# Performance work log

Measured on AMD Instinct MI355X. Metric: run time of the kernel, lower is better.

The kernel has to match this reference:

```python
import jax, jax.numpy as jnp
import numpy as np

PSZ = 3      # patch_size
TOPK = 2     # topk candidates
EPS = 1e-12  # F.normalize eps


def extract_patches(x, psz, stride):
    """Torch unfold-style patch extraction: (B,C,H,W) -> (B, nH*nW, C, psz, psz)."""
    B, C, H, W = x.shape
    nH = (H - psz) // stride + 1
    nW = (W - psz) // stride + 1
    slices = []
    for di in range(psz):          # fixed 3x3 loop, not a data-dim loop
        for dj in range(psz):
            slices.append(x[:, :, di:di + (nH - 1) * stride + 1:stride,
                                  dj:dj + (nW - 1) * stride + 1:stride])
    p = jnp.stack(slices, axis=-1)                      # (B,C,nH,nW,psz*psz)
    p = p.reshape(B, C, nH, nW, psz, psz)
    p = p.transpose(0, 2, 3, 1, 4, 5).reshape(B, nH * nW, C, psz, psz)
    return p


def l2_normalize(x, axis):
    n = jnp.sqrt(jnp.sum(x * x, axis=axis, keepdims=True))
    return x / jnp.maximum(n, EPS)


def setup_inputs() -> dict:
    key = jax.random.key(0)
    k1, k2 = jax.random.split(key)
    pred_style = jax.random.normal(k1, (2, 128, 48, 48), dtype=jnp.float32)
    target_style = jax.random.normal(k2, (2 * TOPK, 128, 48, 48), dtype=jnp.float32)
    return {"pred_style": pred_style, "target_style": target_style}


def reference(pred_style, target_style):
    B = pred_style.shape[0]
    # raw patches (used for the final MSE / gather)
    tp = extract_patches(target_style, PSZ, 1)   # (B*TOPK, nT, C, 3, 3)
    pp = extract_patches(pred_style, PSZ, 1)     # (B, nQ, C, 3, 3)
    nT = tp.shape[1]

    # matching is done on channel-normalized features (F.normalize dim=1 / dim=2)
    p1n = extract_patches(l2_normalize(pred_style, axis=1), PSZ, 1)  # (B,nQ,C,3,3)
    tpn = l2_normalize(tp, axis=2).reshape(B, TOPK, nT, *tp.shape[2:])

    # cosine cross-correlation == conv with candidate patches as filters
    scores = jnp.einsum('bqcij,bkncij->bknq', p1n, tpn)  # (B,TOPK,nT,nQ)->(B,TOPK,nQ) reduce below

    sv = jnp.max(scores, axis=2)      # (B, TOPK, nQ) best value per candidate set
    si = jnp.argmax(scores, axis=2)   # (B, TOPK, nQ) best spatial idx per k
    k_idx = jnp.argmax(sv, axis=1)    # (B, nQ) best k per query position
    spatial = jnp.take_along_axis(si, k_idx[:, None, :], axis=1)[:, 0]  # (B, nQ)

    tpr = tp.reshape(B, TOPK, nT, *tp.shape[2:])
    bi = jnp.arange(B)[:, None]
    gathered = tpr[bi, k_idx, spatial]  # (B, nQ, C, 3, 3)

    return jnp.mean((pp - gathered) ** 2)
```

## Files before the change

### kernel.cpp

```cpp
#include <hip/hip_runtime.h>
#include <hip/hip_bf16.h>

typedef unsigned short u16;
typedef __attribute__((ext_vector_type(8))) short short8;
typedef __attribute__((ext_vector_type(4))) float f32x4;
typedef __attribute__((ext_vector_type(4))) unsigned int u32x4;

#define CC    128
#define WW    48
#define HW2   2304
#define NHW   46
#define NQ    2116
#define NPIX  2304
#define DSTRIDE ((size_t)NPIX * NPIX + 64)
#define BATCH 2
#define MT    126
#define NTC   254

__device__ __forceinline__ u16 f2bf(float f) {
  union { float f; unsigned u; } x; x.f = f;
  unsigned r = (x.u + 0x7fffu + ((x.u >> 16) & 1u)) >> 16;
  return (u16)r;
}
__device__ __forceinline__ float b2f(u16 v) {
  union { unsigned u; float f; } x; x.u = ((unsigned)v) << 16;
  return x.f;
}

__global__ __launch_bounds__(256) void k_norm(const float* __restrict__ pred,
                                              const float* __restrict__ targ,
                                              u16* __restrict__ PnT, u16* __restrict__ TnT) {
  const int img = blockIdx.y;
  const int p0  = blockIdx.x * 64;
  const int tid = threadIdx.x;
  const float* src = img < 2 ? pred + (size_t)img * CC * HW2
                             : targ + (size_t)(img - 2) * CC * HW2;
  u16* out = img < 2 ? PnT + (size_t)img * NPIX * CC
                     : TnT + (size_t)(img - 2) * NPIX * CC;

  __shared__ float sT[64][129];
  __shared__ float sInv[64];

  #pragma unroll
  for (int it = 0; it < 32; ++it) {
    int idx = it * 256 + tid;
    int c = idx >> 6, p = idx & 63;
    sT[p][c] = src[(size_t)c * HW2 + p0 + p];
  }
  __syncthreads();
  if (tid < 64) {
    float s = 0.f;
    for (int c = 0; c < CC; ++c) { float v = sT[tid][c]; s += v * v; }
    sInv[tid] = 1.0f / fmaxf(sqrtf(s), 1e-12f);
  }
  __syncthreads();
  #pragma unroll
  for (int it = 0; it < 4; ++it) {
    int cid = it * 256 + tid;
    int p = cid >> 4, g = cid & 15;
    int r = p0 + p;
    int sc = (g & ~7) | ((g & 7) ^ (r & 7));
    float inv = sInv[p];
    unsigned pack[4];
    #pragma unroll
    for (int e = 0; e < 8; ++e) {
      float v = sT[p][sc * 8 + e] * inv;
      if ((e & 1) == 0) pack[e >> 1] = (unsigned)f2bf(v);
      else              pack[e >> 1] |= ((unsigned)f2bf(v)) << 16;
    }
    u32x4 o; o.x = pack[0]; o.y = pack[1]; o.z = pack[2]; o.w = pack[3];
    *reinterpret_cast<u32x4*>(out + (size_t)r * CC + g * 8) = o;
  }
}

__global__ __launch_bounds__(512) void k_pixdotH(const u16* __restrict__ PnT, const u16* __restrict__ TnT,
                                                 u16* __restrict__ H) {
  __shared__ u16 buf[49152];
  u16* sA = buf;
  u16* sB = buf + 16384;
  const int nt = blockIdx.x, mt = blockIdx.y, s = blockIdx.z;
  const int tid = threadIdx.x, lane = tid & 63, wid = tid >> 6;
  const int wm = wid >> 2, wn = wid & 3;
  const int r15 = lane & 15, g16 = lane >> 4;
  const int m0 = mt * MT, n0 = nt * NTC;

  const u16* Ab = PnT + (size_t)(s >> 1) * NPIX * CC;
  const u16* Bb = TnT + (size_t)s * NPIX * CC;
  u16* Hs = H + (size_t)s * DSTRIDE;

  #pragma unroll
  for (int i = 0; i < 4; ++i) {
    int sl = i * 512 + tid;
    int row = m0 + (sl >> 4); row = row < 2303 ? row : 2303;
    __builtin_amdgcn_global_load_lds(
      (const __attribute__((address_space(1))) unsigned*)(Ab + (size_t)row * CC + (sl & 15) * 8),
      (__attribute__((address_space(3))) unsigned*)&sA[sl * 8], 16, 0, 0);
  }
  #pragma unroll
  for (int i = 0; i < 8; ++i) {
    int sl = i * 512 + tid;
    int row = n0 + (sl >> 4); row = row < 2303 ? row : 2303;
    __builtin_amdgcn_global_load_lds(
      (const __attribute__((address_space(1))) unsigned*)(Bb + (size_t)row * CC + (sl & 15) * 8),
      (__attribute__((address_space(3))) unsigned*)&sB[sl * 8], 16, 0, 0);
  }

  f32x4 acc[4][4];
  const f32x4 z4 = {0.f, 0.f, 0.f, 0.f};
  #pragma unroll
  for (int i = 0; i < 4; ++i)
    #pragma unroll
    for (int j = 0; j < 4; ++j) acc[i][j] = z4;

  asm volatile("s_waitcnt vmcnt(0)" ::: "memory");
  __builtin_amdgcn_s_barrier();

  const int arow0 = wm * 64 + r15;
  const int brow0 = wn * 64 + r15;
  #pragma unroll
  for (int ks = 0; ks < 4; ++ks) {
    const int c = ks * 4 + g16;
    short8 af[4], bfv[4];
    #pragma unroll
    for (int mi = 0; mi < 4; ++mi) {
      int row = arow0 + mi * 16;
      int gr = m0 + row;
      af[mi] = *reinterpret_cast<const short8*>(
        &sA[row * 128 + (c >> 3) * 64 + (((c & 7) ^ (gr & 7)) * 8)]);
    }
    #pragma unroll
    for (int ni = 0; ni < 4; ++ni) {
      int row = brow0 + ni * 16;
      int gr = n0 + row;
      bfv[ni] = *reinterpret_cast<const short8*>(
        &sB[row * 128 + (c >> 3) * 64 + (((c & 7) ^ (gr & 7)) * 8)]);
    }
    __builtin_amdgcn_s_setprio(1);
    #pragma unroll
    for (int mi = 0; mi < 4; ++mi)
      #pragma unroll
      for (int ni = 0; ni < 4; ++ni)
        acc[mi][ni] = __builtin_amdgcn_mfma_f32_16x16x32_bf16(af[mi], bfv[ni], acc[mi][ni], 0, 0, 0);
    __builtin_amdgcn_s_setprio(0);
  }

  __syncthreads();
  u16* Dt = buf;
  #pragma unroll
  for (int mi = 0; mi < 4; ++mi)
    #pragma unroll
    for (int ni = 0; ni < 4; ++ni) {
      int col = wn * 64 + ni * 16 + r15;
      #pragma unroll
      for (int rg = 0; rg < 4; ++rg) {
        int row = wm * 64 + mi * 16 + g16 * 4 + rg;
        Dt[row * 256 + col] = f2bf(acc[mi][ni][rg]);
      }
    }
  __syncthreads();

  for (int t = tid; t < 4032; t += 512) {
    int rr = t >> 5, c8 = t & 31;
    int grow = m0 + rr;
    if (grow >= 2302) continue;
    int lcol = c8 * 8;
    int lim = 254 - lcol;
    int glim = 2302 - (n0 + lcol);
    lim = lim < glim ? lim : glim;
    if (lim <= 0) continue;
    int base = rr * 256 + lcol;
    short8 a0 = *reinterpret_cast<const short8*>(&Dt[base]);
    short8 b0 = *reinterpret_cast<const short8*>(&Dt[base + 256]);
    short8 b1 = *reinterpret_cast<const short8*>(&Dt[base + 264]);
    short8 c0 = *reinterpret_cast<const short8*>(&Dt[base + 512]);
    short8 c1 = *reinterpret_cast<const short8*>(&Dt[base + 520]);
    short8 s1v = __builtin_shufflevector(b0, b1, 1, 2, 3, 4, 5, 6, 7, 8);
    short8 s2v = __builtin_shufflevector(c0, c1, 2, 3, 4, 5, 6, 7, 8, 9);
    unsigned pack[4];
    #pragma unroll
    for (int e = 0; e < 8; ++e) {
      float f = b2f((u16)a0[e]) + b2f((u16)s1v[e]) + b2f((u16)s2v[e]);
      if ((e & 1) == 0) pack[e >> 1] = (unsigned)f2bf(f);
      else              pack[e >> 1] |= ((unsigned)f2bf(f)) << 16;
    }
    u16* dst = Hs + (size_t)grow * NPIX + n0 + lcol;
    int nd = lim >= 8 ? 4 : ((lim + 1) >> 1);
    #pragma unroll
    for (int d = 0; d < 4; ++d)
      if (d < nd) *reinterpret_cast<unsigned*>(dst + 2 * d) = pack[d];
  }
}

__global__ __launch_bounds__(512) void k_stencil(const u16* __restrict__ H,
                                                 const float* __restrict__ pred,
                                                 const float* __restrict__ targ,
                                                 float* __restrict__ msep) {
  const int bid = blockIdx.x;
  const int b = bid >= NQ ? 1 : 0;
  const int orig = bid - b * NQ;
  const int xcd = orig & 7, pos = orig >> 3;
  const int q = (xcd < 4 ? xcd * 265 : 1060 + (xcd - 4) * 264) + pos;

  const int tid = threadIdx.x, lane = tid & 63, wid = tid >> 6;
  const int qy = q / NHW, qx = q - qy * NHW;
  const int qp = qy * WW + qx;

  float best = -3.0e38f; int bidx = 0x7fffffff;
  #pragma unroll
  for (int it = 0; it < 2; ++it) {
    int t = it * 512 + tid;
    if (t < 552) {
      int kc = t / 276; int rem = t - kc * 276;
      int ny = rem / 6, cx = rem - ny * 6;
      const u16* Hs = H + (size_t)(b * 2 + kc) * DSTRIDE;
      int colb = ny * 48 + cx * 8;
      short8 t0 = *reinterpret_cast<const short8*>(Hs + (size_t)qp * NPIX + colb);
      short8 t1 = *reinterpret_cast<const short8*>(Hs + (size_t)(qp + 48) * NPIX + colb + 48);
      short8 t2 = *reinterpret_cast<const short8*>(Hs + (size_t)(qp + 96) * NPIX + colb + 96);
      int nbase = kc * NQ + ny * NHW + cx * 8;
      #pragma unroll
      for (int e = 0; e < 8; ++e) {
        float sc = b2f((u16)t0[e]) + b2f((u16)t1[e]) + b2f((u16)t2[e]);
        int n = nbase + e;
        bool take = (cx * 8 + e < NHW) &&
                    ((sc > best) || (sc == best && n < bidx));
        best = take ? sc : best;
        bidx = take ? n : bidx;
      }
    }
  }
  #pragma unroll
  for (int off = 1; off < 64; off <<= 1) {
    float ov = __shfl_xor(best, off, 64);
    int   oi = __shfl_xor(bidx, off, 64);
    bool take = (ov > best) || (ov == best && oi < bidx);
    best = take ? ov : best;
    bidx = take ? oi : bidx;
  }

  __shared__ float sv[8]; __shared__ int si[8];
  __shared__ float red[512];
  if (lane == 0) { sv[wid] = best; si[wid] = bidx; }
  __syncthreads();
  float fb = sv[0]; int fi = si[0];
  #pragma unroll
  for (int wv = 1; wv < 8; ++wv) {
    bool take = (sv[wv] > fb) || (sv[wv] == fb && si[wv] < fi);
    fb = take ? sv[wv] : fb;
    fi = take ? si[wv] : fi;
  }

  int nkc = fi >= NQ ? 1 : 0;
  int ns = fi - nkc * NQ;
  int ny = ns / NHW, nx = ns - ny * NHW;
  const float* P = pred + (size_t)b * CC * HW2;
  const float* T = targ + (size_t)(b * 2 + nkc) * CC * HW2;
  float ssum = 0.f;
  for (int i = tid; i < CC * 9; i += 512) {
    int c = i / 9, sp = i - 9 * c;
    int di = sp / 3, dj = sp - 3 * di;
    float d = P[(size_t)c * HW2 + (qy + di) * WW + qx + dj]
            - T[(size_t)c * HW2 + (ny + di) * WW + nx + dj];
    ssum += d * d;
  }
  red[tid] = ssum; __syncthreads();
  for (int st = 256; st > 0; st >>= 1) { if (tid < st) red[tid] += red[tid + st]; __syncthreads(); }
  if (tid == 0) msep[b * NQ + q] = red[0];
}

__global__ void k_final(const float* __restrict__ msep, float* __restrict__ out) {
  int t = threadIdx.x;
  float s = 0.f;
  for (int i = t; i < BATCH * NQ; i += 256) s += msep[i];
  __shared__ float red[256];
  red[t] = s; __syncthreads();
  for (int st = 128; st > 0; st >>= 1) { if (t < st) red[t] += red[t + st]; __syncthreads(); }
  if (t == 0) out[0] = red[0] * (1.0f / 4875264.0f);
}

extern "C" void kernel_launch(void* const* d_in, const int* in_sizes, int n_in,
                              void* d_out, int out_size, void* d_ws, size_t ws_size,
                              hipStream_t stream) {
  const float* pred = (const float*)d_in[0];
  const float* targ = (const float*)d_in[1];
  char* ws = (char*)d_ws;

  size_t offP = 0;
  size_t offT = offP + (size_t)2 * NPIX * CC * 2;
  size_t offH = offT + (size_t)4 * NPIX * CC * 2;
  size_t offM = offH + (size_t)4 * DSTRIDE * 2;

  u16*   PnT  = (u16*)(ws + offP);
  u16*   TnT  = (u16*)(ws + offT);
  u16*   Hbuf = (u16*)(ws + offH);
  float* msep = (float*)(ws + offM);

  k_norm<<<dim3(36, 6), 256, 0, stream>>>(pred, targ, PnT, TnT);
  k_pixdotH<<<dim3(10, 19, 4), 512, 0, stream>>>(PnT, TnT, Hbuf);
  k_stencil<<<dim3(BATCH * NQ), 512, 0, stream>>>(Hbuf, pred, targ, msep);
  k_final<<<1, 256, 0, stream>>>(msep, (float*)d_out);
}
```

Baseline: 77.50 us.

## Shrink pixdot N-tile to fit two blocks per CU; use shuffle reduction in stencil

The pixel-dot GEMM kernel's N tile drops from 254 to 190 columns. Each wave now computes 64x48 instead of 64x64, and LDS use falls from 96KB to 80KB, so with launch_bounds(512,2) two blocks can be resident per CU. The grid grows from 10 to 13 N-tiles, which means more blocks and more halo recomputation, and the edge store count is adjusted. Separately, the stencil kernel's 512-entry LDS tree reduction is replaced by wave shuffles plus an 8-entry combine, removing many barriers.

```diff
diff --git a/kernel.cpp b/kernel.cpp
--- a/kernel.cpp
+++ b/kernel.cpp
@@ -15,7 +15,8 @@
 #define DSTRIDE ((size_t)NPIX * NPIX + 64)
 #define BATCH 2
 #define MT    126
-#define NTC   254
+#define NTC   190
+#define DTS   200
 
 __device__ __forceinline__ u16 f2bf(float f) {
   union { float f; unsigned u; } x; x.f = f;
@@ -73,9 +74,9 @@
   }
 }
 
-__global__ __launch_bounds__(512) void k_pixdotH(const u16* __restrict__ PnT, const u16* __restrict__ TnT,
-                                                 u16* __restrict__ H) {
-  __shared__ u16 buf[49152];
+__global__ __launch_bounds__(512, 2) void k_pixdotH(const u16* __restrict__ PnT, const u16* __restrict__ TnT,
+                                                    u16* __restrict__ H) {
+  __shared__ u16 buf[40960];
   u16* sA = buf;
   u16* sB = buf + 16384;
   const int nt = blockIdx.x, mt = blockIdx.y, s = blockIdx.z;
@@ -97,7 +98,7 @@
       (__attribute__((address_space(3))) unsigned*)&sA[sl * 8], 16, 0, 0);
   }
   #pragma unroll
-  for (int i = 0; i < 8; ++i) {
+  for (int i = 0; i < 6; ++i) {
     int sl = i * 512 + tid;
     int row = n0 + (sl >> 4); row = row < 2303 ? row : 2303;
     __builtin_amdgcn_global_load_lds(
@@ -105,22 +106,22 @@
       (__attribute__((address_space(3))) unsigned*)&sB[sl * 8], 16, 0, 0);
   }
 
-  f32x4 acc[4][4];
+  f32x4 acc[4][3];
   const f32x4 z4 = {0.f, 0.f, 0.f, 0.f};
   #pragma unroll
   for (int i = 0; i < 4; ++i)
     #pragma unroll
-    for (int j = 0; j < 4; ++j) acc[i][j] = z4;
+    for (int j = 0; j < 3; ++j) acc[i][j] = z4;
 
   asm volatile("s_waitcnt vmcnt(0)" ::: "memory");
   __builtin_amdgcn_s_barrier();
 
   const int arow0 = wm * 64 + r15;
-  const int brow0 = wn * 64 + r15;
+  const int brow0 = wn * 48 + r15;
   #pragma unroll
   for (int ks = 0; ks < 4; ++ks) {
     const int c = ks * 4 + g16;
-    short8 af[4], bfv[4];
+    short8 af[4], bfv[3];
     #pragma unroll
     for (int mi = 0; mi < 4; ++mi) {
       int row = arow0 + mi * 16;
@@ -129,7 +130,7 @@
         &sA[row * 128 + (c >> 3) * 64 + (((c & 7) ^ (gr & 7)) * 8)]);
     }
     #pragma unroll
-    for (int ni = 0; ni < 4; ++ni) {
+    for (int ni = 0; ni < 3; ++ni) {
       int row = brow0 + ni * 16;
       int gr = n0 + row;
       bfv[ni] = *reinterpret_cast<const short8*>(
@@ -139,7 +140,7 @@
     #pragma unroll
     for (int mi = 0; mi < 4; ++mi)
       #pragma unroll
-      for (int ni = 0; ni < 4; ++ni)
+      for (int ni = 0; ni < 3; ++ni)
         acc[mi][ni] = __builtin_amdgcn_mfma_f32_16x16x32_bf16(af[mi], bfv[ni], acc[mi][ni], 0, 0, 0);
     __builtin_amdgcn_s_setprio(0);
   }
@@ -149,31 +150,31 @@
   #pragma unroll
   for (int mi = 0; mi < 4; ++mi)
     #pragma unroll
-    for (int ni = 0; ni < 4; ++ni) {
-      int col = wn * 64 + ni * 16 + r15;
+    for (int ni = 0; ni < 3; ++ni) {
+      int col = wn * 48 + ni * 16 + r15;
       #pragma unroll
       for (int rg = 0; rg < 4; ++rg) {
         int row = wm * 64 + mi * 16 + g16 * 4 + rg;
-        Dt[row * 256 + col] = f2bf(acc[mi][ni][rg]);
+        Dt[row * DTS + col] = f2bf(acc[mi][ni][rg]);
       }
     }
   __syncthreads();
 
-  for (int t = tid; t < 4032; t += 512) {
-    int rr = t >> 5, c8 = t & 31;
+  for (int t = tid; t < 126 * 24; t += 512) {
+    int rr = t / 24, c8 = t - rr * 24;
     int grow = m0 + rr;
     if (grow >= 2302) continue;
     int lcol = c8 * 8;
-    int lim = 254 - lcol;
+    int lim = NTC - lcol;
     int glim = 2302 - (n0 + lcol);
     lim = lim < glim ? lim : glim;
     if (lim <= 0) continue;
-    int base = rr * 256 + lcol;
+    int base = rr * DTS + lcol;
     short8 a0 = *reinterpret_cast<const short8*>(&Dt[base]);
-    short8 b0 = *reinterpret_cast<const short8*>(&Dt[base + 256]);
-    short8 b1 = *reinterpret_cast<const short8*>(&Dt[base + 264]);
-    short8 c0 = *reinterpret_cast<const short8*>(&Dt[base + 512]);
-    short8 c1 = *reinterpret_cast<const short8*>(&Dt[base + 520]);
+    short8 b0 = *reinterpret_cast<const short8*>(&Dt[base + DTS]);
+    short8 b1 = *reinterpret_cast<const short8*>(&Dt[base + DTS + 8]);
+    short8 c0 = *reinterpret_cast<const short8*>(&Dt[base + 2 * DTS]);
+    short8 c1 = *reinterpret_cast<const short8*>(&Dt[base + 2 * DTS + 8]);
     short8 s1v = __builtin_shufflevector(b0, b1, 1, 2, 3, 4, 5, 6, 7, 8);
     short8 s2v = __builtin_shufflevector(c0, c1, 2, 3, 4, 5, 6, 7, 8, 9);
     unsigned pack[4];
@@ -184,7 +185,7 @@
       else              pack[e >> 1] |= ((unsigned)f2bf(f)) << 16;
     }
     u16* dst = Hs + (size_t)grow * NPIX + n0 + lcol;
-    int nd = lim >= 8 ? 4 : ((lim + 1) >> 1);
+    int nd = lim >= 8 ? 4 : (lim >> 1);
     #pragma unroll
     for (int d = 0; d < 4; ++d)
       if (d < nd) *reinterpret_cast<unsigned*>(dst + 2 * d) = pack[d];
@@ -239,7 +240,7 @@
   }
 
   __shared__ float sv[8]; __shared__ int si[8];
-  __shared__ float red[512];
+  __shared__ float rsum[8];
   if (lane == 0) { sv[wid] = best; si[wid] = bidx; }
   __syncthreads();
   float fb = sv[0]; int fi = si[0];
@@ -263,9 +264,16 @@
             - T[(size_t)c * HW2 + (ny + di) * WW + nx + dj];
     ssum += d * d;
   }
-  red[tid] = ssum; __syncthreads();
-  for (int st = 256; st > 0; st >>= 1) { if (tid < st) red[tid] += red[tid + st]; __syncthreads(); }
-  if (tid == 0) msep[b * NQ + q] = red[0];
+  #pragma unroll
+  for (int off = 1; off < 64; off <<= 1) ssum += __shfl_xor(ssum, off, 64);
+  if (lane == 0) rsum[wid] = ssum;
+  __syncthreads();
+  if (tid == 0) {
+    float t = 0.f;
+    #pragma unroll
+    for (int wv = 0; wv < 8; ++wv) t += rsum[wv];
+    msep[b * NQ + q] = t;
+  }
 }
 
 __global__ void k_final(const float* __restrict__ msep, float* __restrict__ out) {
@@ -296,7 +304,7 @@
   float* msep = (float*)(ws + offM);
 
   k_norm<<<dim3(36, 6), 256, 0, stream>>>(pred, targ, PnT, TnT);
-  k_pixdotH<<<dim3(10, 19, 4), 512, 0, stream>>>(PnT, TnT, Hbuf);
+  k_pixdotH<<<dim3(13, 19, 4), 512, 0, stream>>>(PnT, TnT, Hbuf);
   k_stencil<<<dim3(BATCH * NQ), 512, 0, stream>>>(Hbuf, pred, targ, msep);
   k_final<<<1, 256, 0, stream>>>(msep, (float*)d_out);
 }
```

Result: faster. 72.60 us (-6.3%).
